# Performance work log

Measured on AMD Instinct MI355X. Metric: run time of the kernel, lower is better.

The kernel has to match this reference:

```python
import jax, jax.numpy as jnp
import numpy as np

N_NODES = 50000
N_EDGES = 1_600_000
IN_DIM, OUT_DIM, N_HEADS = 256, 64, 4
EPS = 1e-12  # F.normalize eps


def setup_inputs() -> dict:
    key = jax.random.key(0)
    k1, k2, k3, k4, k5 = jax.random.split(key, 5)
    h = jax.random.normal(k1, (N_NODES, IN_DIM), dtype=jnp.float32)
    edge_index = jax.random.randint(k2, (2, N_EDGES), 0, N_NODES, dtype=jnp.int32)
    # small scale keeps exp(leaky_relu(.)) well-conditioned (mimics xavier init)
    W = jax.random.normal(k3, (IN_DIM, OUT_DIM), dtype=jnp.float32) * 0.05
    Wl = jax.random.normal(k4, (N_HEADS, OUT_DIM), dtype=jnp.float32) * 0.05
    Wr = jax.random.normal(k5, (N_HEADS, OUT_DIM), dtype=jnp.float32) * 0.05
    b = jnp.zeros((OUT_DIM,), dtype=jnp.float32)
    return {"h": h, "W": W, "Wl": Wl, "Wr": Wr, "b": b, "edge_index": edge_index}


def reference(h, W, Wl, Wr, b, edge_index):
    N = h.shape[0]
    H = Wl.shape[0]
    x = h @ W                      # [N, D]
    el = x @ Wl.T                  # [N, H]
    er = x @ Wr.T                  # [N, H]
    src, dst = edge_index[0], edge_index[1]
    e = el[src] + er[dst]          # [E, H]
    e = jnp.exp(jax.nn.leaky_relu(e, negative_slope=0.2))
    # L1 row normalization over edges == F.normalize(dense_scatter, p=1, dim=-1)
    rowsum = jax.ops.segment_sum(e, src, num_segments=N)          # [N, H]
    w = e / jnp.maximum(rowsum, EPS)[src]                          # [E, H]
    # SpMM aggregation, per head to bound peak memory
    heads = [jax.ops.segment_sum(w[:, hd:hd + 1] * x[dst], src, num_segments=N)
             for hd in range(H)]
    out = jnp.stack(heads, axis=1)                                 # [N, H, D]
    out = jax.nn.elu(out + b)
    return out.reshape(N, H * x.shape[1])                          # [N, H*D]
```

## Files before the change

### kernel.cpp

```cpp
#include <hip/hip_runtime.h>
#include <hip/hip_bf16.h>
#include <hip/hip_fp16.h>

#define N_NODES 50000
#define N_EDGES 1600000
#define NPB    50
#define NBUK   1000
#define NSL    8
#define BCAPS  320
#define BCAPH  1280
#define GEMMB  782
#define PARTB  256
#define CHUNK  6250
#define BD     10

typedef __attribute__((ext_vector_type(8))) short short8;
typedef __attribute__((ext_vector_type(4))) float f32x4;

__device__ __forceinline__ unsigned short f2bf(float f) {
  union { float f; unsigned int i; } v; v.f = f;
  unsigned int i = v.i;
  unsigned int r = i + 0x7FFFu + ((i >> 16) & 1u);
  return (unsigned short)(r >> 16);
}

__global__ __launch_bounds__(256) void k_xpart(const float* __restrict__ hmat,
    const float* __restrict__ Wmat, float* __restrict__ x,
    const int* __restrict__ ei, int* __restrict__ bcnt,
    unsigned int* __restrict__ raw) {
  __shared__ __align__(16) char smem[44032];
  const int t = threadIdx.x;
  if (blockIdx.x < GEMMB) {
    unsigned short* Wt = (unsigned short*)smem;
    for (int idx = t; idx < 64 * 256; idx += 256) {
      int k = idx >> 6, n = idx & 63;
      Wt[n * 264 + k] = f2bf(Wmat[idx]);
    }
    __syncthreads();
    const int wave = t >> 6, lane = t & 63;
    const int quad = lane >> 4, l16 = lane & 15;
    const int m0 = blockIdx.x * 64 + wave * 16;
    int arow = m0 + l16; if (arow >= N_NODES) arow = N_NODES - 1;
    f32x4 c[4] = {{0,0,0,0},{0,0,0,0},{0,0,0,0},{0,0,0,0}};
    const float* aptr = hmat + (size_t)arow * 256 + quad * 8;
    #pragma unroll
    for (int kb = 0; kb < 8; ++kb) {
      f32x4 a0 = *(const f32x4*)(aptr + kb * 32);
      f32x4 a1 = *(const f32x4*)(aptr + kb * 32 + 4);
      short8 a;
      a[0] = (short)f2bf(a0[0]); a[1] = (short)f2bf(a0[1]);
      a[2] = (short)f2bf(a0[2]); a[3] = (short)f2bf(a0[3]);
      a[4] = (short)f2bf(a1[0]); a[5] = (short)f2bf(a1[1]);
      a[6] = (short)f2bf(a1[2]); a[7] = (short)f2bf(a1[3]);
      #pragma unroll
      for (int nt = 0; nt < 4; ++nt) {
        int n = nt * 16 + l16;
        short8 b = *(const short8*)(&Wt[n * 264 + kb * 32 + quad * 8]);
        c[nt] = __builtin_amdgcn_mfma_f32_16x16x32_bf16(a, b, c[nt], 0, 0, 0);
      }
    }
    #pragma unroll
    for (int nt = 0; nt < 4; ++nt) {
      #pragma unroll
      for (int r = 0; r < 4; ++r) {
        int grow = m0 + quad * 4 + r;
        if (grow < N_NODES) x[grow * 64 + nt * 16 + l16] = c[nt][r];
      }
    }
  } else {
    int* scnt = (int*)smem;
    unsigned int* sbin = (unsigned int*)(smem + 4000);
    const int pj = blockIdx.x - GEMMB;
    const int slice = blockIdx.x & 7;
    for (int i = t; i < NBUK; i += 256) scnt[i] = 0;
    __syncthreads();
    const int e0 = pj * CHUNK;
    for (int e = e0 + t; e < e0 + CHUNK; e += 256) {
      int s = ei[e], d = ei[N_EDGES + e];
      int b = s / NPB;
      int sl = s - b * NPB;
      unsigned int val = ((unsigned int)d << 8) | (unsigned int)sl;
      int p = atomicAdd(&scnt[b], 1);
      if (p < BD) {
        sbin[b * BD + p] = val;
      } else {
        int cell = b * NSL + slice;
        int gp = atomicAdd(&bcnt[cell * 16], 1);
        if (gp < BCAPS) raw[(size_t)cell * BCAPS + gp] = val;
      }
    }
    __syncthreads();
    for (int b = t; b < NBUK; b += 256) {
      int c = scnt[b]; if (c > BD) c = BD;
      if (c > 0) {
        int cell = b * NSL + slice;
        int gp = atomicAdd(&bcnt[cell * 16], c);
        for (int k = 0; k < c; ++k) {
          int idx = gp + k;
          if (idx < BCAPS) raw[(size_t)cell * BCAPS + idx] = sbin[b * BD + k];
        }
      }
    }
  }
}

__global__ __launch_bounds__(256) void k_eler(const float* __restrict__ x,
    const float* __restrict__ Wl, const float* __restrict__ Wr,
    float* __restrict__ el, float* __restrict__ er,
    __half* __restrict__ x16) {
  const int lane = threadIdx.x & 63;
  const int gw = (blockIdx.x * 256 + threadIdx.x) >> 6;
  const int nw = gridDim.x * 4;
  float wl[4], wr[4];
  #pragma unroll
  for (int hh = 0; hh < 4; ++hh) {
    wl[hh] = Wl[hh * 64 + lane];
    wr[hh] = Wr[hh * 64 + lane];
  }
  for (int r = gw; r < N_NODES; r += nw) {
    float xv = x[r * 64 + lane];
    x16[r * 64 + lane] = __float2half(xv);
    float p[4], q[4];
    #pragma unroll
    for (int hh = 0; hh < 4; ++hh) { p[hh] = xv * wl[hh]; q[hh] = xv * wr[hh]; }
    #pragma unroll
    for (int off = 32; off > 0; off >>= 1) {
      #pragma unroll
      for (int hh = 0; hh < 4; ++hh) {
        p[hh] += __shfl_xor(p[hh], off, 64);
        q[hh] += __shfl_xor(q[hh], off, 64);
      }
    }
    if (lane == 0) {
      f32x4 pv = {p[0], p[1], p[2], p[3]};
      f32x4 qv = {q[0], q[1], q[2], q[3]};
      ((f32x4*)el)[r] = pv;
      ((f32x4*)er)[r] = qv;
    }
  }
}

__global__ __launch_bounds__(256) void k_bucket(const unsigned int* __restrict__ raw,
    const int* __restrict__ bcnt,
    const float* __restrict__ el, const float* __restrict__ er,
    int4* __restrict__ recs, int* __restrict__ rs_s, int* __restrict__ rs_e) {
  __shared__ unsigned int sraw[BCAPH];
  __shared__ int pref[NPB + 1];
  __shared__ int cur[NPB];
  const int b = blockIdx.x >> 1, H = blockIdx.x & 1, t = threadIdx.x;
  const int s0 = H * 4;
  int c0 = bcnt[(b * NSL + s0 + 0) * 16]; if (c0 > BCAPS) c0 = BCAPS;
  int c1 = bcnt[(b * NSL + s0 + 1) * 16]; if (c1 > BCAPS) c1 = BCAPS;
  int c2 = bcnt[(b * NSL + s0 + 2) * 16]; if (c2 > BCAPS) c2 = BCAPS;
  int c3 = bcnt[(b * NSL + s0 + 3) * 16]; if (c3 > BCAPS) c3 = BCAPS;
  const int o1 = c0, o2 = c0 + c1, o3 = c0 + c1 + c2, cnt = o3 + c3;
  if (t <= NPB) pref[t] = 0;
  __syncthreads();
  for (int j = t; j < c0; j += 256) { unsigned int r = raw[(size_t)(b*NSL+s0+0)*BCAPS + j]; sraw[j]      = r; atomicAdd(&pref[(int)(r & 255u) + 1], 1); }
  for (int j = t; j < c1; j += 256) { unsigned int r = raw[(size_t)(b*NSL+s0+1)*BCAPS + j]; sraw[o1 + j] = r; atomicAdd(&pref[(int)(r & 255u) + 1], 1); }
  for (int j = t; j < c2; j += 256) { unsigned int r = raw[(size_t)(b*NSL+s0+2)*BCAPS + j]; sraw[o2 + j] = r; atomicAdd(&pref[(int)(r & 255u) + 1], 1); }
  for (int j = t; j < c3; j += 256) { unsigned int r = raw[(size_t)(b*NSL+s0+3)*BCAPS + j]; sraw[o3 + j] = r; atomicAdd(&pref[(int)(r & 255u) + 1], 1); }
  __syncthreads();
  if (t == 0) {
    int run = 0;
    #pragma unroll
    for (int n = 0; n <= NPB; ++n) { run += pref[n]; pref[n] = run; }
  }
  __syncthreads();
  const int wbase = (b * 2 + H) * BCAPH;
  if (t < NPB) {
    cur[t] = pref[t];
    rs_s[H * N_NODES + b * NPB + t] = wbase + pref[t];
    rs_e[H * N_NODES + b * NPB + t] = wbase + pref[t + 1];
  }
  __syncthreads();
  const int base = b * NPB;
  for (int j = t; j < cnt; j += 256) {
    unsigned int r = sraw[j];
    int sl = (int)(r & 255u);
    int d  = (int)(r >> 8);
    int pos = atomicAdd(&cur[sl], 1);
    f32x4 a = ((const f32x4*)el)[base + sl];
    f32x4 e = ((const f32x4*)er)[d];
    float w[4];
    #pragma unroll
    for (int hh = 0; hh < 4; ++hh) {
      float tt = a[hh] + e[hh];
      tt = (tt >= 0.f) ? tt : 0.2f * tt;
      w[hh] = __expf(tt);
    }
    union { __half2 h; int i; } u01, u23;
    u01.h = __floats2half2_rn(w[0], w[1]);
    u23.h = __floats2half2_rn(w[2], w[3]);
    int4 rc; rc.x = d; rc.y = u01.i; rc.z = u23.i; rc.w = 0;
    recs[(size_t)wbase + pos] = rc;
  }
}

__global__ __launch_bounds__(256) void k_agg(const __half* __restrict__ x16,
    const int* __restrict__ rs_s, const int* __restrict__ rs_e,
    const int4* __restrict__ recs,
    const float* __restrict__ bvec, float* __restrict__ out) {
  const int node = (blockIdx.x * 256 + threadIdx.x) >> 6;
  const int lane = threadIdx.x & 63;
  if (node >= N_NODES) return;
  float n0 = 0.f, n1 = 0.f, n2 = 0.f, n3 = 0.f;
  float d0 = 0.f, d1 = 0.f, d2 = 0.f, d3 = 0.f;
  #pragma unroll
  for (int hf = 0; hf < 2; ++hf) {
    const int j0 = __builtin_amdgcn_readfirstlane(rs_s[hf * N_NODES + node]);
    const int j1 = __builtin_amdgcn_readfirstlane(rs_e[hf * N_NODES + node]);
    #pragma unroll 4
    for (int j = j0; j < j1; ++j) {
      int4 rec = recs[j];
      union { int i; __half2 h; } u01, u23;
      u01.i = rec.y; u23.i = rec.z;
      float2 f01 = __half22float2(u01.h);
      float2 f23 = __half22float2(u23.h);
      const __half* rowp = x16 + ((size_t)rec.x << 6);
      float xv = __half2float(rowp[lane]);
      d0 += f01.x; d1 += f01.y; d2 += f23.x; d3 += f23.y;
      n0 = fmaf(f01.x, xv, n0); n1 = fmaf(f01.y, xv, n1);
      n2 = fmaf(f23.x, xv, n2); n3 = fmaf(f23.y, xv, n3);
    }
  }
  float bv = bvec[lane];
  size_t ob = (size_t)node * 256 + lane;
  float o;
  o = n0 / fmaxf(d0, 1e-12f) + bv; o = (o > 0.f) ? o : (__expf(o) - 1.f); out[ob      ] = o;
  o = n1 / fmaxf(d1, 1e-12f) + bv; o = (o > 0.f) ? o : (__expf(o) - 1.f); out[ob +  64] = o;
  o = n2 / fmaxf(d2, 1e-12f) + bv; o = (o > 0.f) ? o : (__expf(o) - 1.f); out[ob + 128] = o;
  o = n3 / fmaxf(d3, 1e-12f) + bv; o = (o > 0.f) ? o : (__expf(o) - 1.f); out[ob + 192] = o;
}

extern "C" void kernel_launch(void* const* d_in, const int* in_sizes, int n_in,
                              void* d_out, int out_size, void* d_ws, size_t ws_size,
                              hipStream_t stream) {
  const float* h  = (const float*)d_in[0];
  const float* W  = (const float*)d_in[1];
  const float* Wl = (const float*)d_in[2];
  const float* Wr = (const float*)d_in[3];
  const float* b  = (const float*)d_in[4];
  const int*   ei = (const int*)d_in[5];
  float* out = (float*)d_out;

  char* ws = (char*)d_ws;
  float*        x    = (float*)       (ws + 0);
  float*        el   = (float*)       (ws + 12800000);
  float*        er   = (float*)       (ws + 13600000);
  int*          bcnt = (int*)         (ws + 14400000);
  unsigned int* raw  = (unsigned int*)(ws + 14912000);
  int4*         recs = (int4*)        (ws + 25152000);
  int*          rs_s = (int*)         (ws + 66112000);
  int*          rs_e = (int*)         (ws + 66512000);
  __half*       x16  = (__half*)      (ws + 66912000);
  (void)ws_size; (void)in_sizes; (void)n_in; (void)out_size;

  hipMemsetAsync(bcnt, 0, 512000, stream);

  k_xpart  <<<GEMMB + PARTB, 256, 0, stream>>>(h, W, x, ei, bcnt, raw);
  k_eler   <<<782,   256, 0, stream>>>(x, Wl, Wr, el, er, x16);
  k_bucket <<<2000,  256, 0, stream>>>(raw, bcnt, el, er, recs, rs_s, rs_e);
  k_agg    <<<12500, 256, 0, stream>>>(x16, rs_s, rs_e, recs, b, out);
}
```

Baseline: 263.3 us.

## Fuse bucket sort and aggregation into one kernel using shared-memory CSR

Merges the bucketing and aggregation kernels into a single kernel per bucket of 50 nodes. The sorted edge records and the per-row weight sums now live in shared memory instead of a global records array, which removes the global write and re-read of the 16-byte records and one kernel launch. Row sums are built with shared float atomics, so the aggregation loop no longer accumulates the denominators. The trade-off is fewer, larger blocks (1000 blocks of 512 threads) with about 30KB of shared memory each, which reduces parallelism in the gather phase, and the sums now add in a nondeterministic order.

```diff
diff --git a/kernel.cpp b/kernel.cpp
--- a/kernel.cpp
+++ b/kernel.cpp
@@ -8,7 +8,7 @@
 #define NBUK   1000
 #define NSL    8
 #define BCAPS  320
-#define BCAPH  1280
+#define MAXE   2560
 #define GEMMB  782
 #define PARTB  256
 #define CHUNK  6250
@@ -140,97 +140,104 @@
   }
 }
 
-__global__ __launch_bounds__(256) void k_bucket(const unsigned int* __restrict__ raw,
+__global__ __launch_bounds__(512, 8) void k_bagg(const unsigned int* __restrict__ raw,
     const int* __restrict__ bcnt,
     const float* __restrict__ el, const float* __restrict__ er,
-    int4* __restrict__ recs, int* __restrict__ rs_s, int* __restrict__ rs_e) {
-  __shared__ unsigned int sraw[BCAPH];
+    const __half* __restrict__ x16, const float* __restrict__ bvec,
+    float* __restrict__ out) {
+  __shared__ int dArr[MAXE];
+  __shared__ uint2 hArr[MAXE];
   __shared__ int pref[NPB + 1];
   __shared__ int cur[NPB];
-  const int b = blockIdx.x >> 1, H = blockIdx.x & 1, t = threadIdx.x;
-  const int s0 = H * 4;
-  int c0 = bcnt[(b * NSL + s0 + 0) * 16]; if (c0 > BCAPS) c0 = BCAPS;
-  int c1 = bcnt[(b * NSL + s0 + 1) * 16]; if (c1 > BCAPS) c1 = BCAPS;
-  int c2 = bcnt[(b * NSL + s0 + 2) * 16]; if (c2 > BCAPS) c2 = BCAPS;
-  int c3 = bcnt[(b * NSL + s0 + 3) * 16]; if (c3 > BCAPS) c3 = BCAPS;
-  const int o1 = c0, o2 = c0 + c1, o3 = c0 + c1 + c2, cnt = o3 + c3;
-  if (t <= NPB) pref[t] = 0;
-  __syncthreads();
-  for (int j = t; j < c0; j += 256) { unsigned int r = raw[(size_t)(b*NSL+s0+0)*BCAPS + j]; sraw[j]      = r; atomicAdd(&pref[(int)(r & 255u) + 1], 1); }
-  for (int j = t; j < c1; j += 256) { unsigned int r = raw[(size_t)(b*NSL+s0+1)*BCAPS + j]; sraw[o1 + j] = r; atomicAdd(&pref[(int)(r & 255u) + 1], 1); }
-  for (int j = t; j < c2; j += 256) { unsigned int r = raw[(size_t)(b*NSL+s0+2)*BCAPS + j]; sraw[o2 + j] = r; atomicAdd(&pref[(int)(r & 255u) + 1], 1); }
-  for (int j = t; j < c3; j += 256) { unsigned int r = raw[(size_t)(b*NSL+s0+3)*BCAPS + j]; sraw[o3 + j] = r; atomicAdd(&pref[(int)(r & 255u) + 1], 1); }
-  __syncthreads();
+  __shared__ float rowsum[NPB][4];
+  __shared__ int osl[NSL + 1];
+  const int b = blockIdx.x, t = threadIdx.x;
   if (t == 0) {
     int run = 0;
     #pragma unroll
+    for (int s = 0; s < NSL; ++s) {
+      osl[s] = run;
+      int c = bcnt[(b * NSL + s) * 16]; if (c > BCAPS) c = BCAPS;
+      run += c;
+    }
+    osl[NSL] = run;
+  }
+  if (t <= NPB) pref[t] = 0;
+  if (t < NPB) { rowsum[t][0] = 0.f; rowsum[t][1] = 0.f; rowsum[t][2] = 0.f; rowsum[t][3] = 0.f; }
+  __syncthreads();
+  for (int s = 0; s < NSL; ++s) {
+    const int c = osl[s + 1] - osl[s];
+    for (int j = t; j < c; j += 512) {
+      unsigned int r = raw[(size_t)(b * NSL + s) * BCAPS + j];
+      atomicAdd(&pref[(int)(r & 255u) + 1], 1);
+    }
+  }
+  __syncthreads();
+  if (t == 0) {
+    int run = 0;
+    #pragma unroll
     for (int n = 0; n <= NPB; ++n) { run += pref[n]; pref[n] = run; }
   }
   __syncthreads();
-  const int wbase = (b * 2 + H) * BCAPH;
-  if (t < NPB) {
-    cur[t] = pref[t];
-    rs_s[H * N_NODES + b * NPB + t] = wbase + pref[t];
-    rs_e[H * N_NODES + b * NPB + t] = wbase + pref[t + 1];
-  }
+  if (t < NPB) cur[t] = pref[t];
   __syncthreads();
   const int base = b * NPB;
-  for (int j = t; j < cnt; j += 256) {
-    unsigned int r = sraw[j];
-    int sl = (int)(r & 255u);
-    int d  = (int)(r >> 8);
-    int pos = atomicAdd(&cur[sl], 1);
-    f32x4 a = ((const f32x4*)el)[base + sl];
-    f32x4 e = ((const f32x4*)er)[d];
-    float w[4];
-    #pragma unroll
-    for (int hh = 0; hh < 4; ++hh) {
-      float tt = a[hh] + e[hh];
-      tt = (tt >= 0.f) ? tt : 0.2f * tt;
-      w[hh] = __expf(tt);
-    }
-    union { __half2 h; int i; } u01, u23;
-    u01.h = __floats2half2_rn(w[0], w[1]);
-    u23.h = __floats2half2_rn(w[2], w[3]);
-    int4 rc; rc.x = d; rc.y = u01.i; rc.z = u23.i; rc.w = 0;
-    recs[(size_t)wbase + pos] = rc;
-  }
-}
-
-__global__ __launch_bounds__(256) void k_agg(const __half* __restrict__ x16,
-    const int* __restrict__ rs_s, const int* __restrict__ rs_e,
-    const int4* __restrict__ recs,
-    const float* __restrict__ bvec, float* __restrict__ out) {
-  const int node = (blockIdx.x * 256 + threadIdx.x) >> 6;
-  const int lane = threadIdx.x & 63;
-  if (node >= N_NODES) return;
-  float n0 = 0.f, n1 = 0.f, n2 = 0.f, n3 = 0.f;
-  float d0 = 0.f, d1 = 0.f, d2 = 0.f, d3 = 0.f;
-  #pragma unroll
-  for (int hf = 0; hf < 2; ++hf) {
-    const int j0 = __builtin_amdgcn_readfirstlane(rs_s[hf * N_NODES + node]);
-    const int j1 = __builtin_amdgcn_readfirstlane(rs_e[hf * N_NODES + node]);
+  for (int s = 0; s < NSL; ++s) {
+    const int c = osl[s + 1] - osl[s];
+    for (int j = t; j < c; j += 512) {
+      unsigned int r = raw[(size_t)(b * NSL + s) * BCAPS + j];
+      int sl = (int)(r & 255u);
+      int d  = (int)(r >> 8);
+      f32x4 a = ((const f32x4*)el)[base + sl];
+      f32x4 e = ((const f32x4*)er)[d];
+      float w[4];
+      #pragma unroll
+      for (int hh = 0; hh < 4; ++hh) {
+        float tt = a[hh] + e[hh];
+        tt = (tt >= 0.f) ? tt : 0.2f * tt;
+        w[hh] = __expf(tt);
+      }
+      union { __half2 h; unsigned int i; } u01, u23;
+      u01.h = __floats2half2_rn(w[0], w[1]);
+      u23.h = __floats2half2_rn(w[2], w[3]);
+      float2 w01 = __half22float2(u01.h);
+      float2 w23 = __half22float2(u23.h);
+      int pos = atomicAdd(&cur[sl], 1);
+      dArr[pos] = d;
+      hArr[pos] = make_uint2(u01.i, u23.i);
+      atomicAdd(&rowsum[sl][0], w01.x); atomicAdd(&rowsum[sl][1], w01.y);
+      atomicAdd(&rowsum[sl][2], w23.x); atomicAdd(&rowsum[sl][3], w23.y);
+    }
+  }
+  __syncthreads();
+  const int wv = t >> 6, lane = t & 63;
+  const float bv = bvec[lane];
+  for (int n = wv; n < NPB; n += 8) {
+    const int j0 = __builtin_amdgcn_readfirstlane(pref[n]);
+    const int j1 = __builtin_amdgcn_readfirstlane(pref[n + 1]);
+    float n0 = 0.f, n1 = 0.f, n2 = 0.f, n3 = 0.f;
     #pragma unroll 4
     for (int j = j0; j < j1; ++j) {
-      int4 rec = recs[j];
-      union { int i; __half2 h; } u01, u23;
-      u01.i = rec.y; u23.i = rec.z;
+      const int dd = __builtin_amdgcn_readfirstlane(dArr[j]);
+      uint2 hw = hArr[j];
+      union { unsigned int i; __half2 h; } u01, u23;
+      u01.i = hw.x; u23.i = hw.y;
       float2 f01 = __half22float2(u01.h);
       float2 f23 = __half22float2(u23.h);
-      const __half* rowp = x16 + ((size_t)rec.x << 6);
+      const __half* rowp = x16 + ((size_t)dd << 6);
       float xv = __half2float(rowp[lane]);
-      d0 += f01.x; d1 += f01.y; d2 += f23.x; d3 += f23.y;
       n0 = fmaf(f01.x, xv, n0); n1 = fmaf(f01.y, xv, n1);
       n2 = fmaf(f23.x, xv, n2); n3 = fmaf(f23.y, xv, n3);
     }
-  }
-  float bv = bvec[lane];
-  size_t ob = (size_t)node * 256 + lane;
-  float o;
-  o = n0 / fmaxf(d0, 1e-12f) + bv; o = (o > 0.f) ? o : (__expf(o) - 1.f); out[ob      ] = o;
-  o = n1 / fmaxf(d1, 1e-12f) + bv; o = (o > 0.f) ? o : (__expf(o) - 1.f); out[ob +  64] = o;
-  o = n2 / fmaxf(d2, 1e-12f) + bv; o = (o > 0.f) ? o : (__expf(o) - 1.f); out[ob + 128] = o;
-  o = n3 / fmaxf(d3, 1e-12f) + bv; o = (o > 0.f) ? o : (__expf(o) - 1.f); out[ob + 192] = o;
+    const float d0 = rowsum[n][0], d1 = rowsum[n][1];
+    const float d2 = rowsum[n][2], d3 = rowsum[n][3];
+    size_t ob = (size_t)(base + n) * 256 + lane;
+    float o;
+    o = n0 / fmaxf(d0, 1e-12f) + bv; o = (o > 0.f) ? o : (__expf(o) - 1.f); out[ob      ] = o;
+    o = n1 / fmaxf(d1, 1e-12f) + bv; o = (o > 0.f) ? o : (__expf(o) - 1.f); out[ob +  64] = o;
+    o = n2 / fmaxf(d2, 1e-12f) + bv; o = (o > 0.f) ? o : (__expf(o) - 1.f); out[ob + 128] = o;
+    o = n3 / fmaxf(d3, 1e-12f) + bv; o = (o > 0.f) ? o : (__expf(o) - 1.f); out[ob + 192] = o;
+  }
 }
 
 extern "C" void kernel_launch(void* const* d_in, const int* in_sizes, int n_in,
@@ -250,16 +257,12 @@
   float*        er   = (float*)       (ws + 13600000);
   int*          bcnt = (int*)         (ws + 14400000);
   unsigned int* raw  = (unsigned int*)(ws + 14912000);
-  int4*         recs = (int4*)        (ws + 25152000);
-  int*          rs_s = (int*)         (ws + 66112000);
-  int*          rs_e = (int*)         (ws + 66512000);
-  __half*       x16  = (__half*)      (ws + 66912000);
+  __half*       x16  = (__half*)      (ws + 25152000);
   (void)ws_size; (void)in_sizes; (void)n_in; (void)out_size;
 
   hipMemsetAsync(bcnt, 0, 512000, stream);
 
   k_xpart  <<<GEMMB + PARTB, 256, 0, stream>>>(h, W, x, ei, bcnt, raw);
-  k_eler   <<<782,   256, 0, stream>>>(x, Wl, Wr, el, er, x16);
-  k_bucket <<<2000,  256, 0, stream>>>(raw, bcnt, el, er, recs, rs_s, rs_e);
-  k_agg    <<<12500, 256, 0, stream>>>(x16, rs_s, rs_e, recs, b, out);
-}
+  k_eler   <<<782,  256, 0, stream>>>(x, Wl, Wr, el, er, x16);
+  k_bagg   <<<NBUK, 512, 0, stream>>>(raw, bcnt, el, er, x16, b, out);
+}
```

Measured after the change: 312.3 us. +18.6%, slower.
